# Optimization experiments

Measured on AMD Instinct MI355X. Metric: run time of the kernel, lower is better.

The kernel has to match this reference:

```python
import jax, jax.numpy as jnp
import numpy as np

N, E, D, K = 32768, 16384, 4, 8          # nodes, hyperedges, edges/node, nodes/edge
IN_DIM, OUT_DIM, EDGE_DIM, NUM_HEADS = 128, 128, 64, 8


def setup_inputs() -> dict:
    key = jax.random.key(0)
    ks = jax.random.split(key, 16)
    s_in = 1.0 / np.sqrt(IN_DIM)
    s_out = 1.0 / np.sqrt(OUT_DIM)
    s_edge = 1.0 / np.sqrt(EDGE_DIM)
    return {
        "x": jax.random.normal(ks[0], (N, IN_DIM), jnp.float32),
        "edge_attr": jax.random.normal(ks[1], (E, EDGE_DIM), jnp.float32),
        "node_edges": jax.random.randint(ks[2], (N, D), 0, E),   # hyperedges containing each node
        "edge_nodes": jax.random.randint(ks[3], (E, K), 0, N),   # nodes inside each hyperedge
        "W_lin": jax.random.normal(ks[4], (OUT_DIM, IN_DIM), jnp.float32) * s_in,
        "W_edge": jax.random.normal(ks[5], (OUT_DIM, EDGE_DIM), jnp.float32) * s_edge,
        "Wq": jax.random.normal(ks[6], (OUT_DIM, OUT_DIM), jnp.float32) * s_out,
        "Wk": jax.random.normal(ks[7], (OUT_DIM, OUT_DIM), jnp.float32) * s_out,
        "Wv": jax.random.normal(ks[8], (OUT_DIM, OUT_DIM), jnp.float32) * s_out,
        "bq": jnp.zeros((OUT_DIM,), jnp.float32),
        "bk": jnp.zeros((OUT_DIM,), jnp.float32),
        "bv": jnp.zeros((OUT_DIM,), jnp.float32),
        "Wo": jax.random.normal(ks[9], (OUT_DIM, OUT_DIM), jnp.float32) * s_out,
        "bo": jnp.zeros((OUT_DIM,), jnp.float32),
    }


def reference(x, edge_attr, node_edges, edge_nodes,
              W_lin, W_edge, Wq, Wk, Wv, bq, bk, bv, Wo, bo):
    n, out_dim = x.shape[0], W_lin.shape[0]
    hd = out_dim // NUM_HEADS
    L = node_edges.shape[1] * edge_nodes.shape[1]  # D*K keys per node

    Wh = x @ W_lin.T                               # [N, out]
    We = edge_attr @ W_edge.T                      # [E, out]

    u_idx = edge_nodes[node_edges]                 # [N, D, K] neighbor node ids
    vals = Wh[u_idx]                               # [N, D, K, out]
    keys = vals + We[node_edges][:, :, None, :]    # key = Wh[u] + We[e]
    keys = keys.reshape(n, L, out_dim)
    vals = vals.reshape(n, L, out_dim)

    # torch nn.MultiheadAttention: single query per node (query = Wh[v])
    q = (Wh @ Wq.T + bq).reshape(n, NUM_HEADS, hd)
    k = (keys @ Wk.T + bk).reshape(n, L, NUM_HEADS, hd)
    v = (vals @ Wv.T + bv).reshape(n, L, NUM_HEADS, hd)

    scores = jnp.einsum('nhd,nlhd->nhl', q, k) / jnp.sqrt(jnp.asarray(hd, q.dtype))
    attn = jax.nn.softmax(scores, axis=-1)         # [N, H, L]
    ctx = jnp.einsum('nhl,nlhd->nhd', attn, v).reshape(n, out_dim)
    out = ctx @ Wo.T + bo
    return jax.nn.relu(out)
```

## Files before the change

kernel.cpp:

```cpp
#include <hip/hip_runtime.h>

#define N_NODES 32768
#define N_EDGES 16384
#define DEG 4
#define KPE 8
#define DIM 128
#define EDIM 64

typedef float f32x4 __attribute__((ext_vector_type(4)));
typedef __bf16 bf16x8 __attribute__((ext_vector_type(8)));
typedef unsigned short u16x8 __attribute__((ext_vector_type(8)));

static __device__ __forceinline__ unsigned short f2bf(float f) {
  union { float f; unsigned int u; } v; v.f = f;
  unsigned int r = (v.u + 0x7FFFu + ((v.u >> 16) & 1u)) >> 16;
  return (unsigned short)r;
}
static __device__ __forceinline__ float bflo(unsigned int v) {
  union { unsigned int u; float f; } x; x.u = v << 16; return x.f;
}
static __device__ __forceinline__ float bfhi(unsigned int v) {
  union { unsigned int u; float f; } x; x.u = v & 0xffff0000u; return x.f;
}

__global__ __launch_bounds__(256) void wprep_kernel(
    const float* __restrict__ Wq, const float* __restrict__ Wk,
    const float* __restrict__ Wv, const float* __restrict__ Wlin,
    const float* __restrict__ Wedge, const float* __restrict__ Wo,
    unsigned short* __restrict__ CW, unsigned short* __restrict__ CWE,
    unsigned short* __restrict__ Wob)
{
  int id = blockIdx.x * 256 + threadIdx.x;
  if (id < 384 * 128) {
    int j = id >> 7, i = id & 127;
    const float* wrow; float scale = 1.0f;
    if (j < 128)      { wrow = Wq + j * 128; scale = 0.25f; }
    else if (j < 256) { wrow = Wk + (j - 128) * 128; }
    else              { wrow = Wv + (j - 256) * 128; }
    float s = 0.f;
    for (int m = 0; m < 128; ++m) s += wrow[m] * Wlin[m * 128 + i];
    CW[id] = f2bf(s * scale);
  } else if (id < 384 * 128 + 128 * 64) {
    int id2 = id - 384 * 128; int j = id2 >> 6, t = id2 & 63;
    float s = 0.f;
    for (int m = 0; m < 128; ++m) s += Wk[j * 128 + m] * Wedge[m * 64 + t];
    CWE[id2] = f2bf(s);
  } else if (id < 384 * 128 + 128 * 64 + 128 * 128) {
    int id3 = id - (384 * 128 + 128 * 64);
    Wob[id3] = f2bf(Wo[id3]);
  }
}

__global__ __launch_bounds__(256) void g1_kernel(
    const float* __restrict__ x, const unsigned short* __restrict__ CW,
    const float* __restrict__ bq, const float* __restrict__ bv,
    unsigned short* __restrict__ qb, unsigned short* __restrict__ Kb,
    unsigned short* __restrict__ Vb)
{
  const int wave = threadIdx.x >> 6, lane = threadIdx.x & 63;
  const int r16 = lane & 15, quad = lane >> 4;
  const int m0 = blockIdx.x * 64 + wave * 16;
  const int n0 = blockIdx.y * 64;

  f32x4 acc[4];
  const f32x4 z = {0.f, 0.f, 0.f, 0.f};
  acc[0] = z; acc[1] = z; acc[2] = z; acc[3] = z;

  const float* arow = x + (size_t)(m0 + r16) * DIM + quad * 8;
  #pragma unroll
  for (int kk = 0; kk < 4; ++kk) {
    float4 a0 = *(const float4*)(arow + kk * 32);
    float4 a1 = *(const float4*)(arow + kk * 32 + 4);
    u16x8 au;
    au[0] = f2bf(a0.x); au[1] = f2bf(a0.y); au[2] = f2bf(a0.z); au[3] = f2bf(a0.w);
    au[4] = f2bf(a1.x); au[5] = f2bf(a1.y); au[6] = f2bf(a1.z); au[7] = f2bf(a1.w);
    bf16x8 av = __builtin_bit_cast(bf16x8, au);
    #pragma unroll
    for (int s = 0; s < 4; ++s) {
      u16x8 bu = *(const u16x8*)(CW + (size_t)(n0 + s * 16 + r16) * DIM + kk * 32 + quad * 8);
      acc[s] = __builtin_amdgcn_mfma_f32_16x16x32_bf16(
          av, __builtin_bit_cast(bf16x8, bu), acc[s], 0, 0, 0);
    }
  }

  const int arr = blockIdx.y >> 1;
  const int colbase = (blockIdx.y & 1) * 64;
  unsigned short* dst = arr == 0 ? qb : (arr == 1 ? Kb : Vb);
  #pragma unroll
  for (int s = 0; s < 4; ++s) {
    int j = colbase + s * 16 + r16;
    float bias = arr == 0 ? 0.25f * bq[j] : (arr == 2 ? bv[j] : 0.f);
    #pragma unroll
    for (int r = 0; r < 4; ++r) {
      int m = m0 + quad * 4 + r;
      dst[(size_t)m * DIM + j] = f2bf(acc[s][r] + bias);
    }
  }
}

__global__ __launch_bounds__(256) void g2_kernel(
    const float* __restrict__ ea, const unsigned short* __restrict__ CWE,
    const float* __restrict__ bk, unsigned short* __restrict__ WeKb)
{
  const int wave = threadIdx.x >> 6, lane = threadIdx.x & 63;
  const int r16 = lane & 15, quad = lane >> 4;
  const int m0 = blockIdx.x * 64 + wave * 16;
  const int n0 = blockIdx.y * 64;

  f32x4 acc[4];
  const f32x4 z = {0.f, 0.f, 0.f, 0.f};
  acc[0] = z; acc[1] = z; acc[2] = z; acc[3] = z;

  const float* arow = ea + (size_t)(m0 + r16) * EDIM + quad * 8;
  #pragma unroll
  for (int kk = 0; kk < 2; ++kk) {
    float4 a0 = *(const float4*)(arow + kk * 32);
    float4 a1 = *(const float4*)(arow + kk * 32 + 4);
    u16x8 au;
    au[0] = f2bf(a0.x); au[1] = f2bf(a0.y); au[2] = f2bf(a0.z); au[3] = f2bf(a0.w);
    au[4] = f2bf(a1.x); au[5] = f2bf(a1.y); au[6] = f2bf(a1.z); au[7] = f2bf(a1.w);
    bf16x8 av = __builtin_bit_cast(bf16x8, au);
    #pragma unroll
    for (int s = 0; s < 4; ++s) {
      u16x8 bu = *(const u16x8*)(CWE + (size_t)(n0 + s * 16 + r16) * EDIM + kk * 32 + quad * 8);
      acc[s] = __builtin_amdgcn_mfma_f32_16x16x32_bf16(
          av, __builtin_bit_cast(bf16x8, bu), acc[s], 0, 0, 0);
    }
  }

  #pragma unroll
  for (int s = 0; s < 4; ++s) {
    int j = n0 + s * 16 + r16;
    float bias = bk[j];
    #pragma unroll
    for (int r = 0; r < 4; ++r) {
      int m = m0 + quad * 4 + r;
      WeKb[(size_t)m * DIM + j] = f2bf(acc[s][r] + bias);
    }
  }
}

__global__ __launch_bounds__(256) void attn_kernel(
    const unsigned short* __restrict__ qb, const unsigned short* __restrict__ Kb,
    const unsigned short* __restrict__ Vb, const unsigned short* __restrict__ WeKb,
    const int* __restrict__ nedges, const int* __restrict__ enodes,
    unsigned short* __restrict__ ctxb)
{
  __shared__ float ldsP[4][264];
  __shared__ int ldsU[4][32];
  const int wave = threadIdx.x >> 6, lane = threadIdx.x & 63;
  const int n = blockIdx.x * 4 + wave;
  const int l = lane & 31, half = lane >> 5;

  const int e = nedges[n * DEG + (l >> 3)];
  const int u = enodes[e * KPE + (l & 7)];
  if (half == 0) ldsU[wave][l] = u;

  const uint4* qp = (const uint4*)(qb + (size_t)n * DIM + half * 64);
  const uint4* kp = (const uint4*)(Kb + (size_t)u * DIM + half * 64);
  const uint4* ep = (const uint4*)(WeKb + (size_t)e * DIM + half * 64);

  float s[4] = {0.f, 0.f, 0.f, 0.f};
  #pragma unroll
  for (int ch = 0; ch < 8; ++ch) {
    uint4 qv = qp[ch], kv = kp[ch], ev = ep[ch];
    const int hi = ch >> 1;
    s[hi] = fmaf(bflo(qv.x), bflo(kv.x) + bflo(ev.x), s[hi]);
    s[hi] = fmaf(bfhi(qv.x), bfhi(kv.x) + bfhi(ev.x), s[hi]);
    s[hi] = fmaf(bflo(qv.y), bflo(kv.y) + bflo(ev.y), s[hi]);
    s[hi] = fmaf(bfhi(qv.y), bfhi(kv.y) + bfhi(ev.y), s[hi]);
    s[hi] = fmaf(bflo(qv.z), bflo(kv.z) + bflo(ev.z), s[hi]);
    s[hi] = fmaf(bfhi(qv.z), bfhi(kv.z) + bfhi(ev.z), s[hi]);
    s[hi] = fmaf(bflo(qv.w), bflo(kv.w) + bflo(ev.w), s[hi]);
    s[hi] = fmaf(bfhi(qv.w), bfhi(kv.w) + bfhi(ev.w), s[hi]);
  }

  #pragma unroll
  for (int hi = 0; hi < 4; ++hi) {
    float vmax = s[hi];
    #pragma unroll
    for (int off = 16; off >= 1; off >>= 1)
      vmax = fmaxf(vmax, __shfl_xor(vmax, off, 32));
    float ex = __expf(s[hi] - vmax);
    float sum = ex;
    #pragma unroll
    for (int off = 16; off >= 1; off >>= 1)
      sum += __shfl_xor(sum, off, 32);
    ldsP[wave][(half * 4 + hi) * 33 + l] = ex / sum;
  }
  __syncthreads();

  const int c0 = lane * 2;
  const int h = lane >> 3;
  float a0 = 0.f, a1 = 0.f;
  #pragma unroll 8
  for (int l2 = 0; l2 < 32; ++l2) {
    float pw = ldsP[wave][h * 33 + l2];
    int uu = ldsU[wave][l2];
    unsigned int vv = *(const unsigned int*)(Vb + (size_t)uu * DIM + c0);
    a0 = fmaf(pw, bflo(vv), a0);
    a1 = fmaf(pw, bfhi(vv), a1);
  }
  unsigned int pk = (unsigned int)f2bf(a0) | ((unsigned int)f2bf(a1) << 16);
  *(unsigned int*)(ctxb + (size_t)n * DIM + c0) = pk;
}

__global__ __launch_bounds__(256) void g4_kernel(
    const unsigned short* __restrict__ ctxb, const unsigned short* __restrict__ Wob,
    const float* __restrict__ bo, float* __restrict__ out)
{
  const int wave = threadIdx.x >> 6, lane = threadIdx.x & 63;
  const int r16 = lane & 15, quad = lane >> 4;
  const int m0 = blockIdx.x * 64 + wave * 16;
  const int n0 = blockIdx.y * 64;

  f32x4 acc[4];
  const f32x4 z = {0.f, 0.f, 0.f, 0.f};
  acc[0] = z; acc[1] = z; acc[2] = z; acc[3] = z;

  #pragma unroll
  for (int kk = 0; kk < 4; ++kk) {
    u16x8 au = *(const u16x8*)(ctxb + (size_t)(m0 + r16) * DIM + kk * 32 + quad * 8);
    bf16x8 av = __builtin_bit_cast(bf16x8, au);
    #pragma unroll
    for (int s = 0; s < 4; ++s) {
      u16x8 bu = *(const u16x8*)(Wob + (size_t)(n0 + s * 16 + r16) * DIM + kk * 32 + quad * 8);
      acc[s] = __builtin_amdgcn_mfma_f32_16x16x32_bf16(
          av, __builtin_bit_cast(bf16x8, bu), acc[s], 0, 0, 0);
    }
  }

  #pragma unroll
  for (int s = 0; s < 4; ++s) {
    int j = n0 + s * 16 + r16;
    float bias = bo[j];
    #pragma unroll
    for (int r = 0; r < 4; ++r) {
      int m = m0 + quad * 4 + r;
      float v = acc[s][r] + bias;
      out[(size_t)m * DIM + j] = v > 0.f ? v : 0.f;
    }
  }
}

extern "C" void kernel_launch(void* const* d_in, const int* in_sizes, int n_in,
                              void* d_out, int out_size, void* d_ws, size_t ws_size,
                              hipStream_t stream)
{
  const float* x     = (const float*)d_in[0];
  const float* ea    = (const float*)d_in[1];
  const int* nedges  = (const int*)d_in[2];
  const int* enodes  = (const int*)d_in[3];
  const float* Wlin  = (const float*)d_in[4];
  const float* Wedge = (const float*)d_in[5];
  const float* Wq    = (const float*)d_in[6];
  const float* Wk    = (const float*)d_in[7];
  const float* Wv    = (const float*)d_in[8];
  const float* bq    = (const float*)d_in[9];
  const float* bk    = (const float*)d_in[10];
  const float* bv    = (const float*)d_in[11];
  const float* Wo    = (const float*)d_in[12];
  const float* bo    = (const float*)d_in[13];
  float* out = (float*)d_out;

  unsigned short* wsp = (unsigned short*)d_ws;
  unsigned short* CW   = wsp;  wsp += 384 * 128;
  unsigned short* CWE  = wsp;  wsp += 128 * 64;
  unsigned short* Wob  = wsp;  wsp += 128 * 128;
  unsigned short* qb   = wsp;  wsp += (size_t)N_NODES * DIM;
  unsigned short* Kb   = wsp;  wsp += (size_t)N_NODES * DIM;
  unsigned short* Vb   = wsp;  wsp += (size_t)N_NODES * DIM;
  unsigned short* WeKb = wsp;  wsp += (size_t)N_EDGES * DIM;
  unsigned short* ctxb = wsp;  wsp += (size_t)N_NODES * DIM;

  wprep_kernel<<<dim3(288), dim3(256), 0, stream>>>(Wq, Wk, Wv, Wlin, Wedge, Wo, CW, CWE, Wob);
  g1_kernel<<<dim3(512, 6), dim3(256), 0, stream>>>(x, CW, bq, bv, qb, Kb, Vb);
  g2_kernel<<<dim3(256, 2), dim3(256), 0, stream>>>(ea, CWE, bk, WeKb);
  attn_kernel<<<dim3(8192), dim3(256), 0, stream>>>(qb, Kb, Vb, WeKb, nedges, enodes, ctxb);
  g4_kernel<<<dim3(512, 2), dim3(256), 0, stream>>>(ctxb, Wob, bo, out);
}
```

Baseline: 243.6 us.

## Hoist gathers in attention kernel, use bf16 dot2, fuse g1 column tiles

The attention kernel now issues every gather up front: Q, K and edge-key rows, all 32 neighbour V values, and the neighbour ids loaded as int4 vectors. This exposes more memory-level parallelism than the old serial per-key V loop. Scores use the packed bf16 fdot2 instruction, which replaces the unpack-add-fma chains; the K and edge contributions are now accumulated separately instead of summed first. The g1 kernel converts each x tile once and loops over all six output column groups, cutting redundant x reads and bf16 conversion at the cost of a 6x smaller grid and higher register pressure. The attention kernel also holds about 32 registers for V plus 24 uint4 values, so occupancy may drop.

```diff
diff --git a/kernel.cpp b/kernel.cpp
--- a/kernel.cpp
+++ b/kernel.cpp
@@ -9,6 +9,7 @@
 
 typedef float f32x4 __attribute__((ext_vector_type(4)));
 typedef __bf16 bf16x8 __attribute__((ext_vector_type(8)));
+typedef __bf16 bf16x2 __attribute__((ext_vector_type(2)));
 typedef unsigned short u16x8 __attribute__((ext_vector_type(8)));
 
 static __device__ __forceinline__ unsigned short f2bf(float f) {
@@ -22,6 +23,18 @@
 static __device__ __forceinline__ float bfhi(unsigned int v) {
   union { unsigned int u; float f; } x; x.u = v & 0xffff0000u; return x.f;
 }
+
+#if __has_builtin(__builtin_amdgcn_fdot2_f32_bf16)
+static __device__ __forceinline__ float dot2bf(unsigned int a, unsigned int b, float c) {
+  return __builtin_amdgcn_fdot2_f32_bf16(
+      __builtin_bit_cast(bf16x2, a), __builtin_bit_cast(bf16x2, b), c, false);
+}
+#else
+static __device__ __forceinline__ float dot2bf(unsigned int a, unsigned int b, float c) {
+  c = fmaf(bflo(a), bflo(b), c);
+  return fmaf(bfhi(a), bfhi(b), c);
+}
+#endif
 
 __global__ __launch_bounds__(256) void wprep_kernel(
     const float* __restrict__ Wq, const float* __restrict__ Wk,
@@ -38,11 +51,13 @@
     else if (j < 256) { wrow = Wk + (j - 128) * 128; }
     else              { wrow = Wv + (j - 256) * 128; }
     float s = 0.f;
+    #pragma unroll 8
     for (int m = 0; m < 128; ++m) s += wrow[m] * Wlin[m * 128 + i];
     CW[id] = f2bf(s * scale);
   } else if (id < 384 * 128 + 128 * 64) {
     int id2 = id - 384 * 128; int j = id2 >> 6, t = id2 & 63;
     float s = 0.f;
+    #pragma unroll 8
     for (int m = 0; m < 128; ++m) s += Wk[j * 128 + m] * Wedge[m * 64 + t];
     CWE[id2] = f2bf(s);
   } else if (id < 384 * 128 + 128 * 64 + 128 * 128) {
@@ -60,12 +75,8 @@
   const int wave = threadIdx.x >> 6, lane = threadIdx.x & 63;
   const int r16 = lane & 15, quad = lane >> 4;
   const int m0 = blockIdx.x * 64 + wave * 16;
-  const int n0 = blockIdx.y * 64;
-
-  f32x4 acc[4];
-  const f32x4 z = {0.f, 0.f, 0.f, 0.f};
-  acc[0] = z; acc[1] = z; acc[2] = z; acc[3] = z;
-
+
+  u16x8 av[4];
   const float* arow = x + (size_t)(m0 + r16) * DIM + quad * 8;
   #pragma unroll
   for (int kk = 0; kk < 4; ++kk) {
@@ -74,26 +85,35 @@
     u16x8 au;
     au[0] = f2bf(a0.x); au[1] = f2bf(a0.y); au[2] = f2bf(a0.z); au[3] = f2bf(a0.w);
     au[4] = f2bf(a1.x); au[5] = f2bf(a1.y); au[6] = f2bf(a1.z); au[7] = f2bf(a1.w);
-    bf16x8 av = __builtin_bit_cast(bf16x8, au);
+    av[kk] = au;
+  }
+
+  #pragma unroll
+  for (int g = 0; g < 6; ++g) {
+    f32x4 acc[4];
+    const f32x4 z = {0.f, 0.f, 0.f, 0.f};
+    acc[0] = z; acc[1] = z; acc[2] = z; acc[3] = z;
+    #pragma unroll
+    for (int kk = 0; kk < 4; ++kk) {
+      #pragma unroll
+      for (int s = 0; s < 4; ++s) {
+        u16x8 bu = *(const u16x8*)(CW + (size_t)(g * 64 + s * 16 + r16) * DIM + kk * 32 + quad * 8);
+        acc[s] = __builtin_amdgcn_mfma_f32_16x16x32_bf16(
+            __builtin_bit_cast(bf16x8, av[kk]), __builtin_bit_cast(bf16x8, bu), acc[s], 0, 0, 0);
+      }
+    }
+    const int arr = g >> 1;
+    const int colbase = (g & 1) * 64;
+    unsigned short* dst = arr == 0 ? qb : (arr == 1 ? Kb : Vb);
     #pragma unroll
     for (int s = 0; s < 4; ++s) {
-      u16x8 bu = *(const u16x8*)(CW + (size_t)(n0 + s * 16 + r16) * DIM + kk * 32 + quad * 8);
-      acc[s] = __builtin_amdgcn_mfma_f32_16x16x32_bf16(
-          av, __builtin_bit_cast(bf16x8, bu), acc[s], 0, 0, 0);
-    }
-  }
-
-  const int arr = blockIdx.y >> 1;
-  const int colbase = (blockIdx.y & 1) * 64;
-  unsigned short* dst = arr == 0 ? qb : (arr == 1 ? Kb : Vb);
-  #pragma unroll
-  for (int s = 0; s < 4; ++s) {
-    int j = colbase + s * 16 + r16;
-    float bias = arr == 0 ? 0.25f * bq[j] : (arr == 2 ? bv[j] : 0.f);
-    #pragma unroll
-    for (int r = 0; r < 4; ++r) {
-      int m = m0 + quad * 4 + r;
-      dst[(size_t)m * DIM + j] = f2bf(acc[s][r] + bias);
+      int j = colbase + s * 16 + r16;
+      float bias = arr == 0 ? 0.25f * bq[j] : (arr == 2 ? bv[j] : 0.f);
+      #pragma unroll
+      for (int r = 0; r < 4; ++r) {
+        int m = m0 + quad * 4 + r;
+        dst[(size_t)m * DIM + j] = f2bf(acc[s][r] + bias);
+      }
     }
   }
 }
@@ -146,33 +166,55 @@
     const int* __restrict__ nedges, const int* __restrict__ enodes,
     unsigned short* __restrict__ ctxb)
 {
-  __shared__ float ldsP[4][264];
-  __shared__ int ldsU[4][32];
+  __shared__ __align__(16) float ldsP[4][288];
   const int wave = threadIdx.x >> 6, lane = threadIdx.x & 63;
   const int n = blockIdx.x * 4 + wave;
   const int l = lane & 31, half = lane >> 5;
-
-  const int e = nedges[n * DEG + (l >> 3)];
-  const int u = enodes[e * KPE + (l & 7)];
-  if (half == 0) ldsU[wave][l] = u;
+  const int j = l >> 3, lo8 = l & 7;
+  const int c0 = lane * 2;
+  const int h = lane >> 3;
+
+  int4 e4 = *(const int4*)(nedges + (size_t)n * DEG);
+  int e = (j & 2) ? ((j & 1) ? e4.w : e4.z) : ((j & 1) ? e4.y : e4.x);
+  int u = enodes[(size_t)e * KPE + lo8];
+
+  int uu[32];
+  *(int4*)&uu[0]  = *(const int4*)(enodes + (size_t)e4.x * KPE);
+  *(int4*)&uu[4]  = *(const int4*)(enodes + (size_t)e4.x * KPE + 4);
+  *(int4*)&uu[8]  = *(const int4*)(enodes + (size_t)e4.y * KPE);
+  *(int4*)&uu[12] = *(const int4*)(enodes + (size_t)e4.y * KPE + 4);
+  *(int4*)&uu[16] = *(const int4*)(enodes + (size_t)e4.z * KPE);
+  *(int4*)&uu[20] = *(const int4*)(enodes + (size_t)e4.z * KPE + 4);
+  *(int4*)&uu[24] = *(const int4*)(enodes + (size_t)e4.w * KPE);
+  *(int4*)&uu[28] = *(const int4*)(enodes + (size_t)e4.w * KPE + 4);
 
   const uint4* qp = (const uint4*)(qb + (size_t)n * DIM + half * 64);
   const uint4* kp = (const uint4*)(Kb + (size_t)u * DIM + half * 64);
   const uint4* ep = (const uint4*)(WeKb + (size_t)e * DIM + half * 64);
 
+  uint4 qv[8], kv[8], ev[8];
+  #pragma unroll
+  for (int ch = 0; ch < 8; ++ch) qv[ch] = qp[ch];
+  #pragma unroll
+  for (int ch = 0; ch < 8; ++ch) kv[ch] = kp[ch];
+  #pragma unroll
+  for (int ch = 0; ch < 8; ++ch) ev[ch] = ep[ch];
+
+  unsigned int vv[32];
+  #pragma unroll
+  for (int t = 0; t < 32; ++t)
+    vv[t] = *(const unsigned int*)(Vb + (size_t)uu[t] * DIM + c0);
+
   float s[4] = {0.f, 0.f, 0.f, 0.f};
   #pragma unroll
   for (int ch = 0; ch < 8; ++ch) {
-    uint4 qv = qp[ch], kv = kp[ch], ev = ep[ch];
     const int hi = ch >> 1;
-    s[hi] = fmaf(bflo(qv.x), bflo(kv.x) + bflo(ev.x), s[hi]);
-    s[hi] = fmaf(bfhi(qv.x), bfhi(kv.x) + bfhi(ev.x), s[hi]);
-    s[hi] = fmaf(bflo(qv.y), bflo(kv.y) + bflo(ev.y), s[hi]);
-    s[hi] = fmaf(bfhi(qv.y), bfhi(kv.y) + bfhi(ev.y), s[hi]);
-    s[hi] = fmaf(bflo(qv.z), bflo(kv.z) + bflo(ev.z), s[hi]);
-    s[hi] = fmaf(bfhi(qv.z), bfhi(kv.z) + bfhi(ev.z), s[hi]);
-    s[hi] = fmaf(bflo(qv.w), bflo(kv.w) + bflo(ev.w), s[hi]);
-    s[hi] = fmaf(bfhi(qv.w), bfhi(kv.w) + bfhi(ev.w), s[hi]);
+    float t = s[hi];
+    t = dot2bf(qv[ch].x, kv[ch].x, t); t = dot2bf(qv[ch].x, ev[ch].x, t);
+    t = dot2bf(qv[ch].y, kv[ch].y, t); t = dot2bf(qv[ch].y, ev[ch].y, t);
+    t = dot2bf(qv[ch].z, kv[ch].z, t); t = dot2bf(qv[ch].z, ev[ch].z, t);
+    t = dot2bf(qv[ch].w, kv[ch].w, t); t = dot2bf(qv[ch].w, ev[ch].w, t);
+    s[hi] = t;
   }
 
   #pragma unroll
@@ -186,20 +228,18 @@
     #pragma unroll
     for (int off = 16; off >= 1; off >>= 1)
       sum += __shfl_xor(sum, off, 32);
-    ldsP[wave][(half * 4 + hi) * 33 + l] = ex / sum;
+    ldsP[wave][(half * 4 + hi) * 36 + l] = ex / sum;
   }
   __syncthreads();
 
-  const int c0 = lane * 2;
-  const int h = lane >> 3;
   float a0 = 0.f, a1 = 0.f;
-  #pragma unroll 8
-  for (int l2 = 0; l2 < 32; ++l2) {
-    float pw = ldsP[wave][h * 33 + l2];
-    int uu = ldsU[wave][l2];
-    unsigned int vv = *(const unsigned int*)(Vb + (size_t)uu * DIM + c0);
-    a0 = fmaf(pw, bflo(vv), a0);
-    a1 = fmaf(pw, bfhi(vv), a1);
+  #pragma unroll
+  for (int t = 0; t < 8; ++t) {
+    float4 p4 = *(const float4*)&ldsP[wave][h * 36 + t * 4];
+    a0 = fmaf(p4.x, bflo(vv[t * 4 + 0]), a0); a1 = fmaf(p4.x, bfhi(vv[t * 4 + 0]), a1);
+    a0 = fmaf(p4.y, bflo(vv[t * 4 + 1]), a0); a1 = fmaf(p4.y, bfhi(vv[t * 4 + 1]), a1);
+    a0 = fmaf(p4.z, bflo(vv[t * 4 + 2]), a0); a1 = fmaf(p4.z, bfhi(vv[t * 4 + 2]), a1);
+    a0 = fmaf(p4.w, bflo(vv[t * 4 + 3]), a0); a1 = fmaf(p4.w, bfhi(vv[t * 4 + 3]), a1);
   }
   unsigned int pk = (unsigned int)f2bf(a0) | ((unsigned int)f2bf(a1) << 16);
   *(unsigned int*)(ctxb + (size_t)n * DIM + c0) = pk;
@@ -274,7 +314,7 @@
   unsigned short* ctxb = wsp;  wsp += (size_t)N_NODES * DIM;
 
   wprep_kernel<<<dim3(288), dim3(256), 0, stream>>>(Wq, Wk, Wv, Wlin, Wedge, Wo, CW, CWE, Wob);
-  g1_kernel<<<dim3(512, 6), dim3(256), 0, stream>>>(x, CW, bq, bv, qb, Kb, Vb);
+  g1_kernel<<<dim3(512), dim3(256), 0, stream>>>(x, CW, bq, bv, qb, Kb, Vb);
   g2_kernel<<<dim3(256, 2), dim3(256), 0, stream>>>(ea, CWE, bk, WeKb);
   attn_kernel<<<dim3(8192), dim3(256), 0, stream>>>(qb, Kb, Vb, WeKb, nedges, enodes, ctxb);
   g4_kernel<<<dim3(512, 2), dim3(256), 0, stream>>>(ctxb, Wob, bo, out);
```

After: 230.7 us. 5.3% less time.
